# Performance work log

Measured on AMD Instinct MI355X. Metric: run time of the kernel, lower is better.

## Reference

```python
import jax, jax.numpy as jnp
import numpy as np

B, S, D, H, DH = 2, 2048, 1024, 16, 64
SCALE = float(np.sqrt(DH))
IGNORE = -100000.0


def setup_inputs() -> dict:
    key = jax.random.key(0)
    ks = jax.random.split(key, 9)
    s = 0.02
    return {
        "x": jax.random.normal(ks[0], (B, S, D), dtype=jnp.float32),
        "W_Q": jax.random.normal(ks[1], (H, DH, D), dtype=jnp.float32) * s,
        "W_K": jax.random.normal(ks[2], (H, DH, D), dtype=jnp.float32) * s,
        "W_V": jax.random.normal(ks[3], (H, DH, D), dtype=jnp.float32) * s,
        "W_O": jax.random.normal(ks[4], (H, D, DH), dtype=jnp.float32) * s,
        "b_Q": jax.random.normal(ks[5], (H, DH), dtype=jnp.float32) * s,
        "b_K": jax.random.normal(ks[6], (H, DH), dtype=jnp.float32) * s,
        "b_V": jax.random.normal(ks[7], (H, DH), dtype=jnp.float32) * s,
        "b_O": jax.random.normal(ks[8], (D,), dtype=jnp.float32) * s,
        "mask": jnp.tril(jnp.ones((S, S), dtype=bool)),  # causal, global attn_type
    }


def reference(x, W_Q, W_K, W_V, W_O, b_Q, b_K, b_V, b_O, mask):
    # q,k,v: [batch, pos, head, d_head]
    q = jnp.einsum('ihm,bpm->bpih', W_Q, x) + b_Q
    k = jnp.einsum('ihm,bpm->bpih', W_K, x) + b_K
    v = jnp.einsum('ihm,bpm->bpih', W_V, x) + b_V
    # scores: [batch, head, q_pos, k_pos]
    attn_scores = jnp.einsum('bpih,bqih->bipq', q, k) / SCALE
    attn_scores = jnp.where(mask, attn_scores, IGNORE)
    attn = jax.nn.softmax(attn_scores, axis=-1)
    # z: [batch, q_pos, head, d_head]
    z = jnp.einsum('bpih,biqp->bqih', v, attn)
    out = jnp.einsum('idh,bqih->bqd', W_O, z) + b_O
    return out
```

## Files before the change

kernel.cpp:

```cpp
#include <hip/hip_runtime.h>
#include <stdint.h>

typedef __attribute__((ext_vector_type(8))) short bf16x8;
typedef __attribute__((ext_vector_type(4))) float f32x4;
typedef __attribute__((ext_vector_type(16))) float f32x16;
typedef __attribute__((ext_vector_type(4))) unsigned short us4;

#define LOG2E 1.44269504088896340736f

__device__ __forceinline__ unsigned short f2bf(float f) {
    union { float f; unsigned u; } v; v.f = f;
    unsigned r = v.u + 0x7FFFu + ((v.u >> 16) & 1u);
    return (unsigned short)(r >> 16);
}
__device__ __forceinline__ float bf2f(unsigned short u) {
    return __uint_as_float(((unsigned)u) << 16);
}

__device__ __forceinline__ unsigned cvtpk(float lo, float hi) {
    unsigned r;
    asm("v_cvt_pk_bf16_f32 %0, %1, %2" : "=v"(r) : "v"(lo), "v"(hi));
    return r;
}
__device__ __forceinline__ void plswap(unsigned &a, unsigned &b) {
    asm volatile("v_permlane32_swap_b32 %0, %1" : "+v"(a), "+v"(b));
}

__device__ __forceinline__ void gld16(const void* g, void* l) {
    __builtin_amdgcn_global_load_lds((const __attribute__((address_space(1))) void*)g,
                                     (__attribute__((address_space(3))) void*)l, 16, 0, 0);
}

__global__ void k_cvt(const float* __restrict__ in, unsigned short* __restrict__ out, int n4) {
    int i = blockIdx.x * blockDim.x + threadIdx.x;
    if (i >= n4) return;
    float4 v = ((const float4*)in)[i];
    us4 o; o.x = f2bf(v.x); o.y = f2bf(v.y); o.z = f2bf(v.z); o.w = f2bf(v.w);
    *(us4*)(out + (size_t)i * 4) = o;
}

__global__ void k_cvt3(const float* __restrict__ a, const float* __restrict__ b,
                       const float* __restrict__ cc,
                       unsigned short* __restrict__ oa, unsigned short* __restrict__ ob,
                       unsigned short* __restrict__ oc) {
    const float* in = blockIdx.y == 0 ? a : (blockIdx.y == 1 ? b : cc);
    unsigned short* out = blockIdx.y == 0 ? oa : (blockIdx.y == 1 ? ob : oc);
    int i = blockIdx.x * blockDim.x + threadIdx.x;
    float4 v = ((const float4*)in)[i];
    us4 o; o.x = f2bf(v.x); o.y = f2bf(v.y); o.z = f2bf(v.z); o.w = f2bf(v.w);
    *(us4*)(out + (size_t)i * 4) = o;
}

__global__ void k_cvt_wo(const float* __restrict__ WO, unsigned short* __restrict__ out) {
    int t = blockIdx.x * blockDim.x + threadIdx.x;
    int d = t >> 10, nn = t & 1023, i = nn >> 6, h = nn & 63;
    out[t] = f2bf(WO[(((size_t)i << 10) + d) * 64 + h]);
}

__global__ __launch_bounds__(256) void k_gemm_qkv(
    const unsigned short* __restrict__ Xb,
    const unsigned short* __restrict__ Wq, const unsigned short* __restrict__ Wk,
    const unsigned short* __restrict__ Wv,
    const float* __restrict__ bQ, const float* __restrict__ bK, const float* __restrict__ bV,
    unsigned short* __restrict__ Qb, unsigned short* __restrict__ Kb, unsigned short* __restrict__ VTb)
{
    __shared__ unsigned short As[2][128][64];
    __shared__ unsigned short Bs[2][128][64];
    const int which = blockIdx.z;
    const unsigned short* Wp = which == 0 ? Wq : (which == 1 ? Wk : Wv);
    const int bm = blockIdx.x, bn = blockIdx.y;
    const int t = threadIdx.x, lane = t & 63, wave = t >> 6;
    const int wm = wave >> 1, wn = wave & 1;
    const int l15 = lane & 15, l4 = lane >> 4;
    const int rsw = l15 & 7;

    const int c0 = wave * 64 + lane;
    f32x4 acc[4][4] = {};

    #pragma unroll
    for (int it = 0; it < 4; ++it) {
        int c = it * 256 + c0;
        int row = c >> 3, sl = (c & 7) ^ (row & 7);
        gld16(Xb + ((bm << 7) + row) * 1024 + 0 + sl * 8, (char*)&As[0][0][0] + ((it * 256 + c0) << 4));
        gld16(Wp + ((bn << 7) + row) * 1024 + 0 + sl * 8, (char*)&Bs[0][0][0] + ((it * 256 + c0) << 4));
    }
    __syncthreads();

    int cur = 0;
    for (int ks = 0; ks < 16; ++ks) {
        if (ks < 15) {
            const int k0 = (ks + 1) << 6;
            #pragma unroll
            for (int it = 0; it < 4; ++it) {
                int c = it * 256 + c0;
                int row = c >> 3, sl = (c & 7) ^ (row & 7);
                gld16(Xb + ((bm << 7) + row) * 1024 + k0 + sl * 8, (char*)&As[cur ^ 1][0][0] + ((it * 256 + c0) << 4));
                gld16(Wp + ((bn << 7) + row) * 1024 + k0 + sl * 8, (char*)&Bs[cur ^ 1][0][0] + ((it * 256 + c0) << 4));
            }
        }
        const char* Ab = (const char*)&As[cur][0][0];
        const char* Bb = (const char*)&Bs[cur][0][0];
        #pragma unroll
        for (int kk = 0; kk < 2; ++kk) {
            bf16x8 af[4], bfg[4];
            #pragma unroll
            for (int m = 0; m < 4; ++m)
                af[m] = *(const bf16x8*)(Ab + (wm * 64 + m * 16 + l15) * 128 + (((kk * 4 + l4) ^ rsw) << 4));
            #pragma unroll
            for (int n = 0; n < 4; ++n)
                bfg[n] = *(const bf16x8*)(Bb + (wn * 64 + n * 16 + l15) * 128 + (((kk * 4 + l4) ^ rsw) << 4));
            #pragma unroll
            for (int m = 0; m < 4; ++m)
                #pragma unroll
                for (int n = 0; n < 4; ++n)
                    acc[m][n] = __builtin_amdgcn_mfma_f32_16x16x32_bf16(af[m], bfg[n], acc[m][n], 0, 0, 0);
        }
        __syncthreads();
        cur ^= 1;
    }
    #pragma unroll
    for (int m = 0; m < 4; ++m) {
        #pragma unroll
        for (int n = 0; n < 4; ++n) {
            int col = (bn << 7) + wn * 64 + n * 16 + l15;
            int i = col >> 6, h = col & 63;
            float bias = which == 0 ? bQ[col] : (which == 1 ? bK[col] : bV[col]);
            #pragma unroll
            for (int r = 0; r < 4; ++r) {
                int p = (bm << 7) + wm * 64 + m * 16 + (l4 << 2) + r;
                int b = p >> 11, s = p & 2047;
                float v = acc[m][n][r] + bias;
                if (which == 0)
                    Qb[(((((size_t)b << 4) + i) << 11) + s) * 64 + h] = f2bf(v * (0.125f * LOG2E));
                else if (which == 1)
                    Kb[(((((size_t)b << 4) + i) << 11) + s) * 64 + h] = f2bf(v);
                else
                    VTb[(((((size_t)b << 4) + i) << 6) + h) * 2048 + s] = f2bf(v);
            }
        }
    }
}

__global__ __launch_bounds__(128) void k_attn(
    const unsigned short* __restrict__ Qb, const unsigned short* __restrict__ Kb,
    const unsigned short* __restrict__ VTb,
    unsigned short* __restrict__ Zp, float* __restrict__ Lse)
{
    __shared__ __align__(16) char Lbuf[16384];
    const int id = (int)blockIdx.x;
    const int bi = id & 31;
    const int r = id >> 5;
    const int c = 31 - (r >> 1);
    const int part = r & 1;
    const int n = c + 1, n0 = (n + 1) >> 1;
    const int t0 = part ? n0 : 0, t1 = part ? n : n0;
    const int lane = threadIdx.x & 63, w = threadIdx.x >> 6;
    const int l31 = lane & 31, hi = lane >> 5;
    const unsigned short* Qh = Qb + (size_t)bi * 2048 * 64;
    const char* Khb = (const char*)(Kb + (size_t)bi * 2048 * 64);
    const char* Vhb = (const char*)(VTb + (size_t)bi * 64 * 2048);
    const int q0 = c * 64 + w * 32;
    const int q = q0 + l31;

    bf16x8 qf[4];
    #pragma unroll
    for (int kk = 0; kk < 4; ++kk)
        qf[kk] = *(const bf16x8*)&Qh[(size_t)q * 64 + kk * 16 + hi * 8];

    const int r8 = lane >> 3;
    const int swz = ((lane & 7) * 16) ^ (r8 << 4);
    const int koff = r8 * 128 + swz;
    const int voff = r8 * 4096 + swz;

    const int rsw = (l31 & 7) << 4;
    int kaddr[8];
    #pragma unroll
    for (int i = 0; i < 8; ++i)
        kaddr[i] = (l31 + 32 * (i >> 2)) * 128 + ((32 * (i & 3) + 16 * hi) ^ rsw);
    int vcol[4];
    #pragma unroll
    for (int f = 0; f < 4; ++f)
        vcol[f] = ((f * 32 + 16 * hi) ^ rsw);

    f32x16 za0 = {}, za1 = {};
    float m_run = -1e30f, l_run = 0.f;

    if (t0 < t1) {
        if (w == 0) {
            const char* src = Khb + (size_t)t0 * 8192 + koff;
            #pragma unroll
            for (int it = 0; it < 8; ++it) gld16(src + it * 1024, &Lbuf[0] + it * 1024);
        } else {
            const char* src = Vhb + (size_t)t0 * 128 + voff;
            #pragma unroll
            for (int it = 0; it < 8; ++it) gld16(src + it * 32768, &Lbuf[8192] + it * 1024);
        }
    }

    for (int t = t0; t < t1; ++t) {
        __syncthreads();
        const char* KL = &Lbuf[0];
        const char* VL = &Lbuf[8192];
        bf16x8 ka[8];
        #pragma unroll
        for (int i = 0; i < 8; ++i) ka[i] = *(const bf16x8*)(KL + kaddr[i]);
        bf16x8 vf0[4], vf1[4];
        #pragma unroll
        for (int f = 0; f < 4; ++f) {
            vf0[f] = *(const bf16x8*)(VL + l31 * 128 + vcol[f]);
            vf1[f] = *(const bf16x8*)(VL + (l31 + 32) * 128 + vcol[f]);
        }
        __syncthreads();
        if (t + 1 < t1) {
            if (w == 0) {
                const char* src = Khb + (size_t)(t + 1) * 8192 + koff;
                #pragma unroll
                for (int it = 0; it < 8; ++it) gld16(src + it * 1024, &Lbuf[0] + it * 1024);
            } else {
                const char* src = Vhb + (size_t)(t + 1) * 128 + voff;
                #pragma unroll
                for (int it = 0; it < 8; ++it) gld16(src + it * 32768, &Lbuf[8192] + it * 1024);
            }
        }

        const bool full = !(t == c && w == 0);
        f32x16 s0 = {}, s1;
        __builtin_amdgcn_s_setprio(1);
        #pragma unroll
        for (int kk = 0; kk < 4; ++kk)
            s0 = __builtin_amdgcn_mfma_f32_32x32x16_bf16(ka[kk], qf[kk], s0, 0, 0, 0);
        if (full) {
            f32x16 z = {};
            #pragma unroll
            for (int kk = 0; kk < 4; ++kk)
                z = __builtin_amdgcn_mfma_f32_32x32x16_bf16(ka[4 + kk], qf[kk], z, 0, 0, 0);
            s1 = z;
        }
        __builtin_amdgcn_s_setprio(0);

        if (!full) {
            #pragma unroll
            for (int j = 0; j < 16; ++j) s1[j] = -100000.0f;
        }
        if (t == c) {
            #pragma unroll
            for (int j = 0; j < 16; ++j) {
                int kv0 = (j & 3) + 8 * (j >> 2) + 4 * hi;
                if (c * 64 + kv0 > q) s0[j] = -100000.0f;
                if (c * 64 + kv0 + 32 > q) s1[j] = -100000.0f;
            }
        }
        float tmax = -1e30f;
        #pragma unroll
        for (int j = 0; j < 16; ++j) tmax = fmaxf(tmax, fmaxf(s0[j], s1[j]));
        tmax = fmaxf(tmax, __shfl_xor(tmax, 32, 64));
        if (!__all(tmax <= m_run + 8.0f)) {
            float newm = fmaxf(m_run, tmax);
            float alpha = exp2f(m_run - newm);
            m_run = newm;
            l_run *= alpha;
            za0 *= alpha; za1 *= alpha;
        }
        float rsum = 0.f;
        #pragma unroll
        for (int j = 0; j < 16; ++j) { s0[j] = exp2f(s0[j] - m_run); rsum += s0[j]; }
        if (full) {
            #pragma unroll
            for (int j = 0; j < 16; ++j) { s1[j] = exp2f(s1[j] - m_run); rsum += s1[j]; }
        }
        rsum += __shfl_xor(rsum, 32, 64);
        l_run += rsum;

        union { unsigned u[4]; bf16x8 v; } pk0, pk1, pk2, pk3;
        {
            unsigned a0 = cvtpk(s0[0], s0[1]),  a1 = cvtpk(s0[2], s0[3]);
            unsigned a2 = cvtpk(s0[4], s0[5]),  a3 = cvtpk(s0[6], s0[7]);
            plswap(a0, a2); plswap(a1, a3);
            pk0.u[0] = a0; pk0.u[1] = a1; pk0.u[2] = a2; pk0.u[3] = a3;
            unsigned b0 = cvtpk(s0[8], s0[9]),  b1 = cvtpk(s0[10], s0[11]);
            unsigned b2 = cvtpk(s0[12], s0[13]), b3 = cvtpk(s0[14], s0[15]);
            plswap(b0, b2); plswap(b1, b3);
            pk1.u[0] = b0; pk1.u[1] = b1; pk1.u[2] = b2; pk1.u[3] = b3;
        }
        if (full) {
            unsigned a0 = cvtpk(s1[0], s1[1]),  a1 = cvtpk(s1[2], s1[3]);
            unsigned a2 = cvtpk(s1[4], s1[5]),  a3 = cvtpk(s1[6], s1[7]);
            plswap(a0, a2); plswap(a1, a3);
            pk2.u[0] = a0; pk2.u[1] = a1; pk2.u[2] = a2; pk2.u[3] = a3;
            unsigned b0 = cvtpk(s1[8], s1[9]),  b1 = cvtpk(s1[10], s1[11]);
            unsigned b2 = cvtpk(s1[12], s1[13]), b3 = cvtpk(s1[14], s1[15]);
            plswap(b0, b2); plswap(b1, b3);
            pk3.u[0] = b0; pk3.u[1] = b1; pk3.u[2] = b2; pk3.u[3] = b3;
        }
        __builtin_amdgcn_s_setprio(1);
        za0 = __builtin_amdgcn_mfma_f32_32x32x16_bf16(vf0[0], pk0.v, za0, 0, 0, 0);
        za1 = __builtin_amdgcn_mfma_f32_32x32x16_bf16(vf1[0], pk0.v, za1, 0, 0, 0);
        za0 = __builtin_amdgcn_mfma_f32_32x32x16_bf16(vf0[1], pk1.v, za0, 0, 0, 0);
        za1 = __builtin_amdgcn_mfma_f32_32x32x16_bf16(vf1[1], pk1.v, za1, 0, 0, 0);
        if (full) {
            za0 = __builtin_amdgcn_mfma_f32_32x32x16_bf16(vf0[2], pk2.v, za0, 0, 0, 0);
            za1 = __builtin_amdgcn_mfma_f32_32x32x16_bf16(vf1[2], pk2.v, za1, 0, 0, 0);
            za0 = __builtin_amdgcn_mfma_f32_32x32x16_bf16(vf0[3], pk3.v, za0, 0, 0, 0);
            za1 = __builtin_amdgcn_mfma_f32_32x32x16_bf16(vf1[3], pk3.v, za1, 0, 0, 0);
        }
        __builtin_amdgcn_s_setprio(0);
    }

    const float rl = (l_run > 0.f) ? 1.0f / l_run : 0.f;
    const float lse = (l_run > 0.f) ? m_run + log2f(l_run) : -1e30f;
    const int pb = (part << 5) + bi;
    unsigned short* zp = Zp + ((size_t)pb * 2048 + q) * 64;
    #pragma unroll
    for (int nn = 0; nn < 2; ++nn) {
        #pragma unroll
        for (int gg = 0; gg < 4; ++gg) {
            int dh0 = nn * 32 + 8 * gg + 4 * hi;
            us4 o;
            float v0 = (nn ? za1[4 * gg + 0] : za0[4 * gg + 0]) * rl;
            float v1 = (nn ? za1[4 * gg + 1] : za0[4 * gg + 1]) * rl;
            float v2 = (nn ? za1[4 * gg + 2] : za0[4 * gg + 2]) * rl;
            float v3 = (nn ? za1[4 * gg + 3] : za0[4 * gg + 3]) * rl;
            o.x = f2bf(v0); o.y = f2bf(v1); o.z = f2bf(v2); o.w = f2bf(v3);
            *(us4*)(zp + dh0) = o;
        }
    }
    if (hi == 0) Lse[(size_t)pb * 2048 + q] = lse;
}

__global__ __launch_bounds__(256) void k_combine(
    const unsigned short* __restrict__ Zp, const float* __restrict__ Lse,
    unsigned short* __restrict__ Zb)
{
    const int tid = blockIdx.x * 256 + threadIdx.x;
    const int dc = tid & 7, q = (tid >> 3) & 2047, bi = tid >> 14;
    const float l0 = Lse[(size_t)bi * 2048 + q];
    const float l1 = Lse[(size_t)(32 + bi) * 2048 + q];
    const float M = fmaxf(l0, l1);
    float e0 = exp2f(l0 - M), e1 = exp2f(l1 - M);
    const float rs = 1.0f / (e0 + e1);
    e0 *= rs; e1 *= rs;
    const size_t base = ((size_t)bi * 2048 + q) * 64 + dc * 8;
    bf16x8 z0 = *(const bf16x8*)(Zp + base);
    bf16x8 z1 = *(const bf16x8*)(Zp + (size_t)32 * 2048 * 64 + base);
    const int b = bi >> 4, ih = bi & 15;
    unsigned short* op = Zb + (((size_t)b * 2048 + q) << 10) + ih * 64 + dc * 8;
    bf16x8 o;
    #pragma unroll
    for (int j = 0; j < 8; ++j) {
        float v = e0 * bf2f((unsigned short)z0[j]) + e1 * bf2f((unsigned short)z1[j]);
        o[j] = (short)f2bf(v);
    }
    *(bf16x8*)op = o;
}

__global__ __launch_bounds__(256) void k_gemm_out(
    const unsigned short* __restrict__ Zb, const unsigned short* __restrict__ Wo,
    const float* __restrict__ bO, float* __restrict__ out)
{
    __shared__ unsigned short As[2][128][64];
    __shared__ unsigned short Bs[2][128][64];
    const int bm = blockIdx.x, bn = blockIdx.y;
    const int t = threadIdx.x, lane = t & 63, wave = t >> 6;
    const int wm = wave >> 1, wn = wave & 1;
    const int l15 = lane & 15, l4 = lane >> 4;
    const int rsw = l15 & 7;
    const int c0 = wave * 64 + lane;
    f32x4 acc[4][4] = {};

    #pragma unroll
    for (int it = 0; it < 4; ++it) {
        int c = it * 256 + c0;
        int row = c >> 3, sl = (c & 7) ^ (row & 7);
        gld16(Zb + ((bm << 7) + row) * 1024 + 0 + sl * 8, (char*)&As[0][0][0] + ((it * 256 + c0) << 4));
        gld16(Wo + ((bn << 7) + row) * 1024 + 0 + sl * 8, (char*)&Bs[0][0][0] + ((it * 256 + c0) << 4));
    }
    __syncthreads();

    int cur = 0;
    for (int ks = 0; ks < 16; ++ks) {
        if (ks < 15) {
            const int k0 = (ks + 1) << 6;
            #pragma unroll
            for (int it = 0; it < 4; ++it) {
                int c = it * 256 + c0;
                int row = c >> 3, sl = (c & 7) ^ (row & 7);
                gld16(Zb + ((bm << 7) + row) * 1024 + k0 + sl * 8, (char*)&As[cur ^ 1][0][0] + ((it * 256 + c0) << 4));
                gld16(Wo + ((bn << 7) + row) * 1024 + k0 + sl * 8, (char*)&Bs[cur ^ 1][0][0] + ((it * 256 + c0) << 4));
            }
        }
        const char* Ab = (const char*)&As[cur][0][0];
        const char* Bb = (const char*)&Bs[cur][0][0];
        #pragma unroll
        for (int kk = 0; kk < 2; ++kk) {
            bf16x8 af[4], bfg[4];
            #pragma unroll
            for (int m = 0; m < 4; ++m)
                af[m] = *(const bf16x8*)(Ab + (wm * 64 + m * 16 + l15) * 128 + (((kk * 4 + l4) ^ rsw) << 4));
            #pragma unroll
            for (int n = 0; n < 4; ++n)
                bfg[n] = *(const bf16x8*)(Bb + (wn * 64 + n * 16 + l15) * 128 + (((kk * 4 + l4) ^ rsw) << 4));
            #pragma unroll
            for (int m = 0; m < 4; ++m)
                #pragma unroll
                for (int n = 0; n < 4; ++n)
                    acc[m][n] = __builtin_amdgcn_mfma_f32_16x16x32_bf16(af[m], bfg[n], acc[m][n], 0, 0, 0);
        }
        __syncthreads();
        cur ^= 1;
    }
    #pragma unroll
    for (int m = 0; m < 4; ++m) {
        #pragma unroll
        for (int n = 0; n < 4; ++n) {
            int col = (bn << 7) + wn * 64 + n * 16 + l15;
            float bias = bO[col];
            #pragma unroll
            for (int r = 0; r < 4; ++r) {
                int p = (bm << 7) + wm * 64 + m * 16 + (l4 << 2) + r;
                out[(size_t)p * 1024 + col] = acc[m][n][r] + bias;
            }
        }
    }
}

extern "C" void kernel_launch(void* const* d_in, const int* in_sizes, int n_in,
                              void* d_out, int out_size, void* d_ws, size_t ws_size,
                              hipStream_t stream)
{
    const float* x  = (const float*)d_in[0];
    const float* WQ = (const float*)d_in[1];
    const float* WK = (const float*)d_in[2];
    const float* WV = (const float*)d_in[3];
    const float* WO = (const float*)d_in[4];
    const float* bQ = (const float*)d_in[5];
    const float* bK = (const float*)d_in[6];
    const float* bV = (const float*)d_in[7];
    const float* bO = (const float*)d_in[8];
    float* out = (float*)d_out;

    char* w = (char*)d_ws;
    unsigned short* xb  = (unsigned short*)w; w += (size_t)4096 * 1024 * 2;
    unsigned short* wqb = (unsigned short*)w; w += (size_t)1024 * 1024 * 2;
    unsigned short* wkb = (unsigned short*)w; w += (size_t)1024 * 1024 * 2;
    unsigned short* wvb = (unsigned short*)w; w += (size_t)1024 * 1024 * 2;
    unsigned short* wob = (unsigned short*)w; w += (size_t)1024 * 1024 * 2;
    unsigned short* Qb  = (unsigned short*)w; w += (size_t)4096 * 1024 * 2;
    unsigned short* Kb  = (unsigned short*)w; w += (size_t)4096 * 1024 * 2;
    unsigned short* VTb = (unsigned short*)w; w += (size_t)4096 * 1024 * 2;
    unsigned short* Zb  = (unsigned short*)w; w += (size_t)4096 * 1024 * 2;
    unsigned short* Zp  = (unsigned short*)w; w += (size_t)2 * 32 * 2048 * 64 * 2;
    float*          Lse = (float*)w;          w += (size_t)2 * 32 * 2048 * 4;

    k_cvt<<<4096, 256, 0, stream>>>(x, xb, 1048576);
    k_cvt3<<<dim3(1024, 3), 256, 0, stream>>>(WQ, WK, WV, wqb, wkb, wvb);
    k_cvt_wo<<<4096, 256, 0, stream>>>(WO, wob);

    k_gemm_qkv<<<dim3(32, 8, 3), 256, 0, stream>>>(xb, wqb, wkb, wvb, bQ, bK, bV, Qb, Kb, VTb);
    k_attn<<<2048, 128, 0, stream>>>(Qb, Kb, VTb, Zp, Lse);
    k_combine<<<2048, 256, 0, stream>>>(Zp, Lse, Zb);
    k_gemm_out<<<dim3(32, 8), 256, 0, stream>>>(Zb, wob, bO, out);
}
```

Measured before the change: 138.5 us.

## Interleave global loads with MFMA and use partial vmcnt waits in projection GEMMs

Both the QKV and output projection GEMMs are restructured. Global-to-LDS staging of the next K tile is now split into four chunks interleaved with the per-row-block MFMA groups. The full __syncthreads is replaced with a raw barrier preceded by s_waitcnt vmcnt(2), so only the current tile's loads must be finished. B fragments are loaded once per K step and s_setprio raises priority around the MFMA bursts. The aim is to hide load latency and barrier stalls behind matrix math, at the cost of relying on exact vmcnt counting; the last iteration redundantly reloads a tile.

```diff
diff --git a/kernel.cpp b/kernel.cpp
--- a/kernel.cpp
+++ b/kernel.cpp
@@ -56,6 +56,12 @@
     int d = t >> 10, nn = t & 1023, i = nn >> 6, h = nn & 63;
     out[t] = f2bf(WO[(((size_t)i << 10) + d) * 64 + h]);
 }
+
+#define STAGE_CHUNK(PTR, BASEROW, K0, IT0, DST) \
+  { int c_ = (IT0) * 256 + c0; int row_ = c_ >> 3, sl_ = (c_ & 7) ^ (row_ & 7); \
+    gld16((PTR) + ((BASEROW) + row_) * 1024 + (K0) + sl_ * 8, (char*)(DST) + (c_ << 4)); \
+    int c2_ = (IT0 + 1) * 256 + c0; int row2_ = c2_ >> 3, sl2_ = (c2_ & 7) ^ (row2_ & 7); \
+    gld16((PTR) + ((BASEROW) + row2_) * 1024 + (K0) + sl2_ * 8, (char*)(DST) + (c2_ << 4)); }
 
 __global__ __launch_bounds__(256) void k_gemm_qkv(
     const unsigned short* __restrict__ Xb,
@@ -73,50 +79,50 @@
     const int wm = wave >> 1, wn = wave & 1;
     const int l15 = lane & 15, l4 = lane >> 4;
     const int rsw = l15 & 7;
-
     const int c0 = wave * 64 + lane;
+    const int arow = bm << 7, brow = bn << 7;
     f32x4 acc[4][4] = {};
 
-    #pragma unroll
-    for (int it = 0; it < 4; ++it) {
-        int c = it * 256 + c0;
-        int row = c >> 3, sl = (c & 7) ^ (row & 7);
-        gld16(Xb + ((bm << 7) + row) * 1024 + 0 + sl * 8, (char*)&As[0][0][0] + ((it * 256 + c0) << 4));
-        gld16(Wp + ((bn << 7) + row) * 1024 + 0 + sl * 8, (char*)&Bs[0][0][0] + ((it * 256 + c0) << 4));
-    }
-    __syncthreads();
-
-    int cur = 0;
+    STAGE_CHUNK(Xb, arow, 0, 0, &As[0][0][0]);
+    STAGE_CHUNK(Xb, arow, 0, 2, &As[0][0][0]);
+    STAGE_CHUNK(Wp, brow, 0, 0, &Bs[0][0][0]);
+    STAGE_CHUNK(Wp, brow, 0, 2, &Bs[0][0][0]);
+
     for (int ks = 0; ks < 16; ++ks) {
-        if (ks < 15) {
-            const int k0 = (ks + 1) << 6;
-            #pragma unroll
-            for (int it = 0; it < 4; ++it) {
-                int c = it * 256 + c0;
-                int row = c >> 3, sl = (c & 7) ^ (row & 7);
-                gld16(Xb + ((bm << 7) + row) * 1024 + k0 + sl * 8, (char*)&As[cur ^ 1][0][0] + ((it * 256 + c0) << 4));
-                gld16(Wp + ((bn << 7) + row) * 1024 + k0 + sl * 8, (char*)&Bs[cur ^ 1][0][0] + ((it * 256 + c0) << 4));
-            }
-        }
+        const int cur = ks & 1, nxt = cur ^ 1;
+        const int k1 = (ks < 15 ? ks + 1 : ks) << 6;
         const char* Ab = (const char*)&As[cur][0][0];
         const char* Bb = (const char*)&Bs[cur][0][0];
-        #pragma unroll
-        for (int kk = 0; kk < 2; ++kk) {
-            bf16x8 af[4], bfg[4];
-            #pragma unroll
-            for (int m = 0; m < 4; ++m)
-                af[m] = *(const bf16x8*)(Ab + (wm * 64 + m * 16 + l15) * 128 + (((kk * 4 + l4) ^ rsw) << 4));
-            #pragma unroll
-            for (int n = 0; n < 4; ++n)
-                bfg[n] = *(const bf16x8*)(Bb + (wn * 64 + n * 16 + l15) * 128 + (((kk * 4 + l4) ^ rsw) << 4));
-            #pragma unroll
-            for (int m = 0; m < 4; ++m)
+        bf16x8 bfg[4][2];
+        #pragma unroll
+        for (int q = 0; q < 4; ++q) {
+            if (q == 0)      { STAGE_CHUNK(Xb, arow, k1, 0, &As[nxt][0][0]); }
+            else if (q == 1) { STAGE_CHUNK(Xb, arow, k1, 2, &As[nxt][0][0]); }
+            else if (q == 2) { STAGE_CHUNK(Wp, brow, k1, 0, &Bs[nxt][0][0]); }
+            else             { STAGE_CHUNK(Wp, brow, k1, 2, &Bs[nxt][0][0]); }
+            if (q == 0) {
+                asm volatile("s_waitcnt vmcnt(2)" ::: "memory");
+                __builtin_amdgcn_s_barrier();
+                asm volatile("" ::: "memory");
                 #pragma unroll
                 for (int n = 0; n < 4; ++n)
-                    acc[m][n] = __builtin_amdgcn_mfma_f32_16x16x32_bf16(af[m], bfg[n], acc[m][n], 0, 0, 0);
-        }
-        __syncthreads();
-        cur ^= 1;
+                    #pragma unroll
+                    for (int kk = 0; kk < 2; ++kk)
+                        bfg[n][kk] = *(const bf16x8*)(Bb + (wn * 64 + n * 16 + l15) * 128 + (((kk * 4 + l4) ^ rsw) << 4));
+            }
+            bf16x8 af0 = *(const bf16x8*)(Ab + (wm * 64 + q * 16 + l15) * 128 + (((0 + l4) ^ rsw) << 4));
+            bf16x8 af1 = *(const bf16x8*)(Ab + (wm * 64 + q * 16 + l15) * 128 + (((4 + l4) ^ rsw) << 4));
+            __builtin_amdgcn_s_setprio(1);
+            #pragma unroll
+            for (int n = 0; n < 4; ++n)
+                acc[q][n] = __builtin_amdgcn_mfma_f32_16x16x32_bf16(af0, bfg[n][0], acc[q][n], 0, 0, 0);
+            #pragma unroll
+            for (int n = 0; n < 4; ++n)
+                acc[q][n] = __builtin_amdgcn_mfma_f32_16x16x32_bf16(af1, bfg[n][1], acc[q][n], 0, 0, 0);
+            __builtin_amdgcn_s_setprio(0);
+        }
+        __builtin_amdgcn_s_barrier();
+        asm volatile("" ::: "memory");
     }
     #pragma unroll
     for (int m = 0; m < 4; ++m) {
@@ -365,48 +371,49 @@
     const int l15 = lane & 15, l4 = lane >> 4;
     const int rsw = l15 & 7;
     const int c0 = wave * 64 + lane;
+    const int arow = bm << 7, brow = bn << 7;
     f32x4 acc[4][4] = {};
 
-    #pragma unroll
-    for (int it = 0; it < 4; ++it) {
-        int c = it * 256 + c0;
-        int row = c >> 3, sl = (c & 7) ^ (row & 7);
-        gld16(Zb + ((bm << 7) + row) * 1024 + 0 + sl * 8, (char*)&As[0][0][0] + ((it * 256 + c0) << 4));
-        gld16(Wo + ((bn << 7) + row) * 1024 + 0 + sl * 8, (char*)&Bs[0][0][0] + ((it * 256 + c0) << 4));
-    }
-    __syncthreads();
-
-    int cur = 0;
+    STAGE_CHUNK(Zb, arow, 0, 0, &As[0][0][0]);
+    STAGE_CHUNK(Zb, arow, 0, 2, &As[0][0][0]);
+    STAGE_CHUNK(Wo, brow, 0, 0, &Bs[0][0][0]);
+    STAGE_CHUNK(Wo, brow, 0, 2, &Bs[0][0][0]);
+
     for (int ks = 0; ks < 16; ++ks) {
-        if (ks < 15) {
-            const int k0 = (ks + 1) << 6;
-            #pragma unroll
-            for (int it = 0; it < 4; ++it) {
-                int c = it * 256 + c0;
-                int row = c >> 3, sl = (c & 7) ^ (row & 7);
-                gld16(Zb + ((bm << 7) + row) * 1024 + k0 + sl * 8, (char*)&As[cur ^ 1][0][0] + ((it * 256 + c0) << 4));
-                gld16(Wo + ((bn << 7) + row) * 1024 + k0 + sl * 8, (char*)&Bs[cur ^ 1][0][0] + ((it * 256 + c0) << 4));
-            }
-        }
+        const int cur = ks & 1, nxt = cur ^ 1;
+        const int k1 = (ks < 15 ? ks + 1 : ks) << 6;
         const char* Ab = (const char*)&As[cur][0][0];
         const char* Bb = (const char*)&Bs[cur][0][0];
-        #pragma unroll
-        for (int kk = 0; kk < 2; ++kk) {
-            bf16x8 af[4], bfg[4];
-            #pragma unroll
-            for (int m = 0; m < 4; ++m)
-                af[m] = *(const bf16x8*)(Ab + (wm * 64 + m * 16 + l15) * 128 + (((kk * 4 + l4) ^ rsw) << 4));
-            #pragma unroll
-            for (int n = 0; n < 4; ++n)
-                bfg[n] = *(const bf16x8*)(Bb + (wn * 64 + n * 16 + l15) * 128 + (((kk * 4 + l4) ^ rsw) << 4));
-            #pragma unroll
-            for (int m = 0; m < 4; ++m)
+        bf16x8 bfg[4][2];
+        #pragma unroll
+        for (int q = 0; q < 4; ++q) {
+            if (q == 0)      { STAGE_CHUNK(Zb, arow, k1, 0, &As[nxt][0][0]); }
+            else if (q == 1) { STAGE_CHUNK(Zb, arow, k1, 2, &As[nxt][0][0]); }
+            else if (q == 2) { STAGE_CHUNK(Wo, brow, k1, 0, &Bs[nxt][0][0]); }
+            else             { STAGE_CHUNK(Wo, brow, k1, 2, &Bs[nxt][0][0]); }
+            if (q == 0) {
+                asm volatile("s_waitcnt vmcnt(2)" ::: "memory");
+                __builtin_amdgcn_s_barrier();
+                asm volatile("" ::: "memory");
                 #pragma unroll
                 for (int n = 0; n < 4; ++n)
-                    acc[m][n] = __builtin_amdgcn_mfma_f32_16x16x32_bf16(af[m], bfg[n], acc[m][n], 0, 0, 0);
-        }
-        __syncthreads();
-        cur ^= 1;
+                    #pragma unroll
+                    for (int kk = 0; kk < 2; ++kk)
+                        bfg[n][kk] = *(const bf16x8*)(Bb + (wn * 64 + n * 16 + l15) * 128 + (((kk * 4 + l4) ^ rsw) << 4));
+            }
+            bf16x8 af0 = *(const bf16x8*)(Ab + (wm * 64 + q * 16 + l15) * 128 + (((0 + l4) ^ rsw) << 4));
+            bf16x8 af1 = *(const bf16x8*)(Ab + (wm * 64 + q * 16 + l15) * 128 + (((4 + l4) ^ rsw) << 4));
+            __builtin_amdgcn_s_setprio(1);
+            #pragma unroll
+            for (int n = 0; n < 4; ++n)
+                acc[q][n] = __builtin_amdgcn_mfma_f32_16x16x32_bf16(af0, bfg[n][0], acc[q][n], 0, 0, 0);
+            #pragma unroll
+            for (int n = 0; n < 4; ++n)
+                acc[q][n] = __builtin_amdgcn_mfma_f32_16x16x32_bf16(af1, bfg[n][1], acc[q][n], 0, 0, 0);
+            __builtin_amdgcn_s_setprio(0);
+        }
+        __builtin_amdgcn_s_barrier();
+        asm volatile("" ::: "memory");
     }
     #pragma unroll
     for (int m = 0; m < 4; ++m) {
```

After: 170.1 us. 1.23x slower.
